# Optimization experiments

Hardware: AMD Instinct MI355X
Metric: run time of the kernel (lower is better)

The kernel has to match this reference:

```python
import jax, jax.numpy as jnp
import numpy as np

EPS = 1e-6

def _rmsnorm(x, w):
    var = jnp.mean(x * x, axis=-1, keepdims=True)
    return w * (x * jax.lax.rsqrt(var + EPS))

def _rope(t, cos, sin):
    # t: [B,S,H,d_k]; cos/sin: [S,d_k/2] -> complex multiply on (even,odd) pairs
    B, S, H, D = t.shape
    tr = t.reshape(B, S, H, D // 2, 2)
    t0, t1 = tr[..., 0], tr[..., 1]
    c = cos[None, :, None, :]
    s = sin[None, :, None, :]
    o0 = t0 * c - t1 * s
    o1 = t0 * s + t1 * c
    return jnp.stack([o0, o1], axis=-1).reshape(B, S, H, D)

def setup_inputs() -> dict:
    key = jax.random.key(0)
    ks = jax.random.split(key, 9)
    B, S, D, H, DFF = 1, 4096, 1024, 16, 4096
    dk = D // H
    hidden = int(2 * DFF / 3)  # 2730, SwiGLU hidden dim
    sc = 0.02
    x = jax.random.normal(ks[0], (B, S, D), jnp.float32)
    # RoPE tables (theta=10000)
    inv_freq = 1.0 / (10000.0 ** (np.arange(0, dk, 2, dtype=np.float32) / dk))
    ang = np.outer(np.arange(S, dtype=np.float32), inv_freq)
    freqs_cos = jnp.asarray(np.cos(ang))
    freqs_sin = jnp.asarray(np.sin(ang))
    # causal additive mask [1,1,S,S]
    mask = jnp.where(np.tril(np.ones((S, S), bool)), 0.0, -1e9).astype(jnp.float32)[None, None]
    Wq = jax.random.normal(ks[1], (D, D), jnp.float32) * sc
    Wk = jax.random.normal(ks[2], (D, D), jnp.float32) * sc
    Wv = jax.random.normal(ks[3], (D, D), jnp.float32) * sc
    Wo = jax.random.normal(ks[4], (D, D), jnp.float32) * sc
    ln1_w = jnp.ones((D,), jnp.float32)
    ln2_w = jnp.ones((D,), jnp.float32)
    w1 = jax.random.normal(ks[5], (D, hidden), jnp.float32) * sc
    w2 = jax.random.normal(ks[6], (hidden, D), jnp.float32) * sc
    w3 = jax.random.normal(ks[7], (D, hidden), jnp.float32) * sc
    return dict(x=x, freqs_cos=freqs_cos, freqs_sin=freqs_sin, mask=mask,
                Wq=Wq, Wk=Wk, Wv=Wv, Wo=Wo, ln1_w=ln1_w, ln2_w=ln2_w,
                w1=w1, w2=w2, w3=w3)

def reference(x, freqs_cos, freqs_sin, mask, Wq, Wk, Wv, Wo, ln1_w, ln2_w, w1, w2, w3):
    B, S, D = x.shape
    H = 16
    dk = D // H
    scale = jnp.sqrt(jnp.float32(dk))
    # attention sublayer (pre-RMSNorm)
    h = _rmsnorm(x, ln1_w)
    Q = (h @ Wq).reshape(B, S, H, dk)
    K = (h @ Wk).reshape(B, S, H, dk)
    V = (h @ Wv).reshape(B, S, H, dk)
    Q = _rope(Q, freqs_cos, freqs_sin)
    K = _rope(K, freqs_cos, freqs_sin)
    scores = jnp.einsum('bshd,bthd->bhst', Q, K) / scale + mask  # [B,H,S,S]
    attn = jax.nn.softmax(scores, axis=-1)
    ctx = jnp.einsum('bhst,bthd->bshd', attn, V).reshape(B, S, D)
    x = x + ctx @ Wo
    # SwiGLU FFN sublayer
    h2 = _rmsnorm(x, ln2_w)
    ff = (jax.nn.silu(h2 @ w1) * (h2 @ w3)) @ w2
    x = x + ff
    return x
```

## Files before the change

kernel.cpp:

```cpp
#include <hip/hip_runtime.h>

#define S_LEN 4096
#define D_MODEL 1024
#define NHEAD 16
#define DK 64
#define HID 2730
#define HIDP 2880
#define QKV_LD 3072

typedef unsigned short u16;
typedef unsigned int u32;
typedef __bf16 bf16x8 __attribute__((ext_vector_type(8)));
typedef float f32x4 __attribute__((ext_vector_type(4)));

#define MFMA16 __builtin_amdgcn_mfma_f32_16x16x32_bf16
#define EXP2 __builtin_amdgcn_exp2f

__device__ __forceinline__ float b2f(u16 u) {
    return __builtin_bit_cast(float, (u32)u << 16);
}
__device__ __forceinline__ u16 f2b(float f) {
    u32 u = __builtin_bit_cast(u32, f);
    u += 0x7FFF + ((u >> 16) & 1);
    return (u16)(u >> 16);
}
__device__ __forceinline__ u32 pk_trunc(float lo, float hi) {
    return __builtin_amdgcn_perm(__builtin_bit_cast(u32, hi),
                                 __builtin_bit_cast(u32, lo), 0x07060302u);
}
__device__ __forceinline__ void gll16(const u16* g, u16* l) {
    __builtin_amdgcn_global_load_lds(
        (__attribute__((address_space(1))) void*)(g),
        (__attribute__((address_space(3))) void*)(l),
        16, 0, 0);
}

__global__ __launch_bounds__(256)
void prep_k(const float* s0, const float* s1, const float* s2,
            const float* s3, const float* s4, const float* s5,
            const float* s6, u16* d0, u16* d1, u16* d2, u16* d3,
            u16* d4, u16* d5, u16* d6,
            const float* __restrict__ x, const float* __restrict__ ln1,
            u16* __restrict__ hb) {
    __shared__ float t[32][33];
    __shared__ float red[4];
    const int bid = blockIdx.x;
    const int tid = threadIdx.x;

    if (bid >= 12736) {
        const int row = bid - 12736;
        const float4 v = ((const float4*)(x + (size_t)row * D_MODEL))[tid];
        float ss = v.x * v.x + v.y * v.y + v.z * v.z + v.w * v.w;
        for (int o = 32; o; o >>= 1) ss += __shfl_down(ss, o);
        if ((tid & 63) == 0) red[tid >> 6] = ss;
        __syncthreads();
        const float tot = red[0] + red[1] + red[2] + red[3];
        const float rs = rsqrtf(tot * (1.0f / D_MODEL) + 1e-6f);
        const float4 wv = ((const float4*)ln1)[tid];
        u16* op = hb + (size_t)row * D_MODEL + tid * 4;
        u32 p0 = (u32)f2b(v.x * rs * wv.x) | ((u32)f2b(v.y * rs * wv.y) << 16);
        u32 p1 = (u32)f2b(v.z * rs * wv.z) | ((u32)f2b(v.w * rs * wv.w) << 16);
        uint2 pk; pk.x = p0; pk.y = p1;
        *(uint2*)op = pk;
        return;
    }

    const float* srcs[7] = {s0, s1, s2, s3, s4, s5, s6};
    u16* dsts[7] = {d0, d1, d2, d3, d4, d5, d6};
    const int RR[7] = {1024, 1024, 1024, 1024, 1024, 1024, 2730};
    const int CC[7] = {1024, 1024, 1024, 1024, 2730, 2730, 1024};
    const int OC[7] = {1024, 1024, 1024, 1024, 1024, 1024, 2880};
    const int XD[7] = {32, 32, 32, 32, 32, 32, 90};

    int seg, start;
    if (bid < 4096)      { seg = bid >> 10; start = seg << 10; }
    else if (bid < 6976) { seg = 4; start = 4096; }
    else if (bid < 9856) { seg = 5; start = 6976; }
    else                 { seg = 6; start = 9856; }
    const int local = bid - start;
    const int bx = local % XD[seg], byy = local / XD[seg];
    const float* in = srcs[seg];
    u16* out = dsts[seg];
    const int R = RR[seg], C = CC[seg], outC = OC[seg];

    const int r0 = byy * 32;
    const int c0 = bx * 32;
    const int tx = tid & 31, ty = tid >> 5;
#pragma unroll
    for (int j = 0; j < 4; ++j) {
        int ir = c0 + ty + j * 8;
        int ic = r0 + tx;
        t[ty + j * 8][tx] = (ir < R && ic < C) ? in[(size_t)ir * C + ic] : 0.0f;
    }
    __syncthreads();
#pragma unroll
    for (int j = 0; j < 4; ++j)
        out[(size_t)(r0 + ty + j * 8) * outC + c0 + tx] = f2b(t[tx][ty + j * 8]);
}

__global__ __launch_bounds__(256)
void rmsnorm_k(const float* __restrict__ x, const float* __restrict__ w,
               u16* __restrict__ out) {
    const int row = blockIdx.x;
    const int tid = threadIdx.x;
    const float4 v = ((const float4*)(x + (size_t)row * D_MODEL))[tid];
    float ss = v.x * v.x + v.y * v.y + v.z * v.z + v.w * v.w;
    for (int o = 32; o; o >>= 1) ss += __shfl_down(ss, o);
    __shared__ float red[4];
    if ((tid & 63) == 0) red[tid >> 6] = ss;
    __syncthreads();
    const float tot = red[0] + red[1] + red[2] + red[3];
    const float rs = rsqrtf(tot * (1.0f / D_MODEL) + 1e-6f);
    const float4 wv = ((const float4*)w)[tid];
    u16* op = out + (size_t)row * D_MODEL + tid * 4;
    u32 p0 = (u32)f2b(v.x * rs * wv.x) | ((u32)f2b(v.y * rs * wv.y) << 16);
    u32 p1 = (u32)f2b(v.z * rs * wv.z) | ((u32)f2b(v.w * rs * wv.w) << 16);
    uint2 pk; pk.x = p0; pk.y = p1;
    *(uint2*)op = pk;
}

__global__ __launch_bounds__(256)
void packkv_k(const u16* __restrict__ qkv, const float* __restrict__ fc,
              const float* __restrict__ fs, u16* __restrict__ vt,
              u16* __restrict__ kp) {
    __shared__ u16 t[32][33];
    const int h = blockIdx.z;
    const int t0 = blockIdx.x * 32;
    const int d0 = blockIdx.y * 32;
    const int tx = threadIdx.x, ty = threadIdx.y;
#pragma unroll
    for (int j = 0; j < 4; ++j)
        t[ty + j * 8][tx] =
            qkv[(size_t)(t0 + ty + j * 8) * QKV_LD + 2 * D_MODEL + h * DK + d0 + tx];

    const int id = ty * 32 + tx;
    const int sA = t0 + (id >> 3);
    const int dA = d0 + (id & 7) * 4;
    uint2 kvp = *(const uint2*)(qkv + (size_t)sA * QKV_LD + D_MODEL + h * DK + dA);
    const int fi = sA * 32 + (dA >> 1);
    const float cc0 = fc[fi], ss0 = fs[fi];
    const float cc1 = fc[fi + 1], ss1 = fs[fi + 1];
    auto rpk = [](u32 w, float c, float s) -> u32 {
        const float a = b2f((u16)w), b = b2f((u16)(w >> 16));
        return (u32)f2b(a * c - b * s) | ((u32)f2b(a * s + b * c) << 16);
    };
    kvp.x = rpk(kvp.x, cc0, ss0);
    kvp.y = rpk(kvp.y, cc1, ss1);
    *(uint2*)(kp + ((size_t)h * S_LEN + sA) * DK + dA) = kvp;

    __syncthreads();
#pragma unroll
    for (int j = 0; j < 4; ++j)
        vt[(size_t)h * DK * S_LEN + (size_t)(d0 + ty + j * 8) * S_LEN + t0 + tx] =
            t[tx][ty + j * 8];
}

template <int EPI>
__global__ __launch_bounds__(256)
void gemm128(const u16* __restrict__ A, int lda, const u16* __restrict__ Bt, int ldb,
             void* __restrict__ C, int ldc, int K, const float* __restrict__ resid) {
    const int m0 = blockIdx.y * 128, n0 = blockIdx.x * 128;
    const int tid = threadIdx.x;
    const int wave = tid >> 6, lane = tid & 63;
    const int wr = wave >> 1, wc = wave & 1;
    const int r16 = lane & 15, kq = lane >> 4;

    __shared__ __align__(16) u16 As[128 * 64];
    __shared__ __align__(16) u16 Bs[128 * 64];

    const int srow = tid >> 3;
    const int scol = ((tid & 7) ^ (srow & 7)) * 8;
    const u16* ag0 = A + (size_t)(m0 +  0 + srow) * lda + scol;
    const u16* ag1 = A + (size_t)(m0 + 32 + srow) * lda + scol;
    const u16* ag2 = A + (size_t)(m0 + 64 + srow) * lda + scol;
    const u16* ag3 = A + (size_t)(m0 + 96 + srow) * lda + scol;
    const u16* bg0 = Bt + (size_t)(n0 +  0 + srow) * ldb + scol;
    const u16* bg1 = Bt + (size_t)(n0 + 32 + srow) * ldb + scol;
    const u16* bg2 = Bt + (size_t)(n0 + 64 + srow) * ldb + scol;
    const u16* bg3 = Bt + (size_t)(n0 + 96 + srow) * ldb + scol;
    u16* const ad = As + tid * 8;
    u16* const bd = Bs + tid * 8;

    f32x4 acc[16];
#pragma unroll
    for (int i = 0; i < 16; ++i) acc[i] = f32x4{0.f, 0.f, 0.f, 0.f};

    const int rsw = r16 & 7;
    for (int k0 = 0; k0 < K; k0 += 64) {
        __syncthreads();
        gll16(ag0 + k0, ad);
        gll16(ag1 + k0, ad + 2048);
        gll16(ag2 + k0, ad + 4096);
        gll16(ag3 + k0, ad + 6144);
        gll16(bg0 + k0, bd);
        gll16(bg1 + k0, bd + 2048);
        gll16(bg2 + k0, bd + 4096);
        gll16(bg3 + k0, bd + 6144);
        __syncthreads();
#pragma unroll
        for (int ks = 0; ks < 2; ++ks) {
            const int slot = (((ks << 2) | kq) ^ rsw) * 8;
            bf16x8 af[4], bf[4];
#pragma unroll
            for (int mt = 0; mt < 4; ++mt)
                af[mt] = *(const bf16x8*)&As[(wr * 64 + mt * 16 + r16) * 64 + slot];
#pragma unroll
            for (int nt = 0; nt < 4; ++nt)
                bf[nt] = *(const bf16x8*)&Bs[(wc * 64 + nt * 16 + r16) * 64 + slot];
#pragma unroll
            for (int mt = 0; mt < 4; ++mt)
#pragma unroll
                for (int nt = 0; nt < 4; ++nt)
                    acc[mt * 4 + nt] = MFMA16(af[mt], bf[nt], acc[mt * 4 + nt], 0, 0, 0);
        }
    }

#pragma unroll
    for (int mt = 0; mt < 4; ++mt) {
#pragma unroll
        for (int nt = 0; nt < 4; ++nt) {
            const int col = n0 + wc * 64 + nt * 16 + r16;
#pragma unroll
            for (int j = 0; j < 4; ++j) {
                const int row = m0 + wr * 64 + mt * 16 + kq * 4 + j;
                if (EPI == 0) {
                    ((u16*)C)[(size_t)row * ldc + col] = f2b(acc[mt * 4 + nt][j]);
                } else {
                    ((float*)C)[(size_t)row * ldc + col] =
                        resid[(size_t)row * ldc + col] + acc[mt * 4 + nt][j];
                }
            }
        }
    }
}

__global__ __launch_bounds__(256)
void gemm64r(const u16* __restrict__ A, int lda, const u16* __restrict__ Bt, int ldb,
             float* __restrict__ C, int ldc, int K, const float* __restrict__ resid) {
    const int m0 = blockIdx.y * 128, n0 = blockIdx.x * 64;
    const int tid = threadIdx.x;
    const int wave = tid >> 6, lane = tid & 63;
    const int r16 = lane & 15, kq = lane >> 4;

    __shared__ __align__(16) u16 As[128 * 64];
    __shared__ __align__(16) u16 Bs[64 * 64];

    const int srow = tid >> 3;
    const int scol = ((tid & 7) ^ (srow & 7)) * 8;
    const u16* ag0 = A + (size_t)(m0 +  0 + srow) * lda + scol;
    const u16* ag1 = A + (size_t)(m0 + 32 + srow) * lda + scol;
    const u16* ag2 = A + (size_t)(m0 + 64 + srow) * lda + scol;
    const u16* ag3 = A + (size_t)(m0 + 96 + srow) * lda + scol;
    const u16* bg0 = Bt + (size_t)(n0 +  0 + srow) * ldb + scol;
    const u16* bg1 = Bt + (size_t)(n0 + 32 + srow) * ldb + scol;
    u16* const ad = As + tid * 8;
    u16* const bd = Bs + tid * 8;

    f32x4 acc[8];
#pragma unroll
    for (int i = 0; i < 8; ++i) acc[i] = f32x4{0.f, 0.f, 0.f, 0.f};

    const int rsw = r16 & 7;
    for (int k0 = 0; k0 < K; k0 += 64) {
        __syncthreads();
        gll16(ag0 + k0, ad);
        gll16(ag1 + k0, ad + 2048);
        gll16(ag2 + k0, ad + 4096);
        gll16(ag3 + k0, ad + 6144);
        gll16(bg0 + k0, bd);
        gll16(bg1 + k0, bd + 2048);
        __syncthreads();
#pragma unroll
        for (int ks = 0; ks < 2; ++ks) {
            const int slot = (((ks << 2) | kq) ^ rsw) * 8;
            bf16x8 af[2], bf[4];
#pragma unroll
            for (int mt = 0; mt < 2; ++mt)
                af[mt] = *(const bf16x8*)&As[(wave * 32 + mt * 16 + r16) * 64 + slot];
#pragma unroll
            for (int nt = 0; nt < 4; ++nt)
                bf[nt] = *(const bf16x8*)&Bs[(nt * 16 + r16) * 64 + slot];
#pragma unroll
            for (int mt = 0; mt < 2; ++mt)
#pragma unroll
                for (int nt = 0; nt < 4; ++nt)
                    acc[mt * 4 + nt] = MFMA16(af[mt], bf[nt], acc[mt * 4 + nt], 0, 0, 0);
        }
    }

#pragma unroll
    for (int mt = 0; mt < 2; ++mt)
#pragma unroll
        for (int nt = 0; nt < 4; ++nt) {
            const int col = n0 + nt * 16 + r16;
#pragma unroll
            for (int j = 0; j < 4; ++j) {
                const int row = m0 + wave * 32 + mt * 16 + kq * 4 + j;
                C[(size_t)row * ldc + col] =
                    resid[(size_t)row * ldc + col] + acc[mt * 4 + nt][j];
            }
        }
}

__global__ __launch_bounds__(256, 3)
void gemm_dual96x(const u16* __restrict__ A, int lda,
                  const u16* __restrict__ B1, const u16* __restrict__ B3, int ldb,
                  u16* __restrict__ C, int ldc, int K) {
    const int m0 = blockIdx.y * 128, n0 = blockIdx.x * 96;
    const int tid = threadIdx.x;
    const int wave = tid >> 6, lane = tid & 63;
    const int wr = wave >> 1, wc = wave & 1;
    const int r16 = lane & 15, kq = lane >> 4;

    __shared__ __align__(16) u16 As[128 * 64];
    __shared__ __align__(16) u16 Bs[192 * 64];

    const int srow = tid >> 3;
    const int scol = ((tid & 7) ^ (srow & 7)) * 8;
    const u16* ag0 = A + (size_t)(m0 +  0 + srow) * lda + scol;
    const u16* ag1 = A + (size_t)(m0 + 32 + srow) * lda + scol;
    const u16* ag2 = A + (size_t)(m0 + 64 + srow) * lda + scol;
    const u16* ag3 = A + (size_t)(m0 + 96 + srow) * lda + scol;
    const u16* bg0 = B1 + (size_t)(n0 +  0 + srow) * ldb + scol;
    const u16* bg1 = B1 + (size_t)(n0 + 32 + srow) * ldb + scol;
    const u16* bg2 = B1 + (size_t)(n0 + 64 + srow) * ldb + scol;
    const u16* bg3 = B3 + (size_t)(n0 +  0 + srow) * ldb + scol;
    const u16* bg4 = B3 + (size_t)(n0 + 32 + srow) * ldb + scol;
    const u16* bg5 = B3 + (size_t)(n0 + 64 + srow) * ldb + scol;
    u16* const ad = As + tid * 8;
    u16* const bd = Bs + tid * 8;

    f32x4 acc1[12], acc3[12];
#pragma unroll
    for (int i = 0; i < 12; ++i) {
        acc1[i] = f32x4{0.f, 0.f, 0.f, 0.f};
        acc3[i] = f32x4{0.f, 0.f, 0.f, 0.f};
    }

    const int rsw = r16 & 7;
    for (int k0 = 0; k0 < K; k0 += 64) {
        __syncthreads();
        gll16(ag0 + k0, ad);
        gll16(ag1 + k0, ad + 2048);
        gll16(ag2 + k0, ad + 4096);
        gll16(ag3 + k0, ad + 6144);
        gll16(bg0 + k0, bd);
        gll16(bg1 + k0, bd + 2048);
        gll16(bg2 + k0, bd + 4096);
        gll16(bg3 + k0, bd + 6144);
        gll16(bg4 + k0, bd + 8192);
        gll16(bg5 + k0, bd + 10240);
        __syncthreads();
#pragma unroll
        for (int ks = 0; ks < 2; ++ks) {
            const int slot = (((ks << 2) | kq) ^ rsw) * 8;
            bf16x8 af[4], b1f[3], b3f[3];
#pragma unroll
            for (int mt = 0; mt < 4; ++mt)
                af[mt] = *(const bf16x8*)&As[(wr * 64 + mt * 16 + r16) * 64 + slot];
#pragma unroll
            for (int nt = 0; nt < 3; ++nt) {
                b1f[nt] = *(const bf16x8*)&Bs[(wc * 48 + nt * 16 + r16) * 64 + slot];
                b3f[nt] = *(const bf16x8*)&Bs[(96 + wc * 48 + nt * 16 + r16) * 64 + slot];
            }
#pragma unroll
            for (int mt = 0; mt < 4; ++mt)
#pragma unroll
                for (int nt = 0; nt < 3; ++nt) {
                    acc1[mt * 3 + nt] = MFMA16(af[mt], b1f[nt], acc1[mt * 3 + nt], 0, 0, 0);
                    acc3[mt * 3 + nt] = MFMA16(af[mt], b3f[nt], acc3[mt * 3 + nt], 0, 0, 0);
                }
        }
    }

#pragma unroll
    for (int mt = 0; mt < 4; ++mt)
#pragma unroll
        for (int nt = 0; nt < 3; ++nt) {
            const int col = n0 + wc * 48 + nt * 16 + r16;
#pragma unroll
            for (int j = 0; j < 4; ++j) {
                const int row = m0 + wr * 64 + mt * 16 + kq * 4 + j;
                const float v1 = acc1[mt * 3 + nt][j];
                const float v3 = acc3[mt * 3 + nt][j];
                const float sig = 1.0f / (1.0f + __expf(-v1));
                C[(size_t)row * ldc + col] = f2b(v1 * sig * v3);
            }
        }
}

__global__ __launch_bounds__(256)
void flash_k(const u16* __restrict__ qkv, const u16* __restrict__ vt,
             const u16* __restrict__ kp, const float* __restrict__ fc,
             const float* __restrict__ fs, u16* __restrict__ ctx) {
    const int h = blockIdx.x;
    const int pair = blockIdx.y;
    const int qa = pair, qb = 63 - pair;
    const int tid = threadIdx.x;
    const int wave = tid >> 6, lane = tid & 63;
    const int r16 = lane & 15, kq = lane >> 4;

    __shared__ __align__(16) u16 Kb[2][2 * 64 * 64];
    __shared__ __align__(16) u16 Vb[2][2 * 64 * 64];
    __shared__ __align__(16) u16 PsB[4 * 16 * 64];
    __shared__ __align__(16) u16 PsA[4 * 16 * 64];

    const u16* kb = kp + (size_t)h * S_LEN * DK;
    const u16* vb = vt + (size_t)h * DK * S_LEN;
    const int srow = tid >> 3;
    const int lcol = ((tid & 7) ^ (srow & 7)) * 8;
    const int qloc = wave * 16 + r16;
    const int sw = r16 & 7;
    const int c0 = (kq ^ sw) * 8;
    const int c1 = ((4 ^ kq) ^ sw) * 8;
    const int psw = r16 & 14;
    u16* psB = PsB + wave * 1024 + r16 * 64;
    u16* psA = PsA + wave * 1024 + r16 * 64;

    const float SC = 0.125f * 1.44269504f;
    auto rp = [SC](u32 w, float c, float s) -> u32 {
        const float a = b2f((u16)w), b = b2f((u16)(w >> 16));
        return (u32)f2b((a * c - b * s) * SC) |
               ((u32)f2b((a * s + b * c) * SC) << 16);
    };
    auto loadq = [&](int qglob, bf16x8& q0out, bf16x8& q1out) {
        const u16* qrow = qkv + (size_t)qglob * QKV_LD + h * DK;
        uint4 uq0 = *(const uint4*)(qrow + kq * 8);
        uint4 uq1 = *(const uint4*)(qrow + 32 + kq * 8);
        const float4 c0v = *(const float4*)(fc + qglob * 32 + kq * 4);
        const float4 s0v = *(const float4*)(fs + qglob * 32 + kq * 4);
        const float4 c1v = *(const float4*)(fc + qglob * 32 + 16 + kq * 4);
        const float4 s1v = *(const float4*)(fs + qglob * 32 + 16 + kq * 4);
        uq0.x = rp(uq0.x, c0v.x, s0v.x); uq0.y = rp(uq0.y, c0v.y, s0v.y);
        uq0.z = rp(uq0.z, c0v.z, s0v.z); uq0.w = rp(uq0.w, c0v.w, s0v.w);
        uq1.x = rp(uq1.x, c1v.x, s1v.x); uq1.y = rp(uq1.y, c1v.y, s1v.y);
        uq1.z = rp(uq1.z, c1v.z, s1v.z); uq1.w = rp(uq1.w, c1v.w, s1v.w);
        q0out = __builtin_bit_cast(bf16x8, uq0);
        q1out = __builtin_bit_cast(bf16x8, uq1);
    };
    const int qgA = qa * 64 + qloc;
    const int qgB = qb * 64 + qloc;
    bf16x8 qfA0, qfA1, qfB0, qfB1;
    loadq(qgA, qfA0, qfA1);
    loadq(qgB, qfB0, qfB1);

    f32x4 oA[4], oB[4];
#pragma unroll
    for (int i = 0; i < 4; ++i) {
        oA[i] = f32x4{0.f, 0.f, 0.f, 0.f};
        oB[i] = f32x4{0.f, 0.f, 0.f, 0.f};
    }
    f32x4 laccA = f32x4{0.f, 0.f, 0.f, 0.f};
    f32x4 laccB = f32x4{0.f, 0.f, 0.f, 0.f};
    const uint4 uone = make_uint4(0x3F803F80u, 0x3F803F80u, 0x3F803F80u, 0x3F803F80u);
    const bf16x8 ones = __builtin_bit_cast(bf16x8, uone);

    auto tile_single = [&](const u16* Ks, const u16* Vs, bool dmask) {
        f32x4 s[4];
#pragma unroll
        for (int nt = 0; nt < 4; ++nt) {
            s[nt] = f32x4{0.f, 0.f, 0.f, 0.f};
            const bf16x8 k0 = *(const bf16x8*)&Ks[(nt * 16 + r16) * 64 + c0];
            s[nt] = MFMA16(k0, qfB0, s[nt], 0, 0, 0);
            const bf16x8 k1 = *(const bf16x8*)&Ks[(nt * 16 + r16) * 64 + c1];
            s[nt] = MFMA16(k1, qfB1, s[nt], 0, 0, 0);
        }
        float pr[16];
#pragma unroll
        for (int nt = 0; nt < 4; ++nt)
#pragma unroll
            for (int j = 0; j < 4; ++j) pr[nt * 4 + j] = EXP2(s[nt][j]);
        if (dmask) {
#pragma unroll
            for (int nt = 0; nt < 4; ++nt)
#pragma unroll
                for (int j = 0; j < 4; ++j)
                    if ((nt * 16 + kq * 4 + j) > qloc) pr[nt * 4 + j] = 0.f;
        }
#pragma unroll
        for (int nt = 0; nt < 4; ++nt) {
            uint2 pk;
            pk.x = pk_trunc(pr[nt * 4 + 0], pr[nt * 4 + 1]);
            pk.y = pk_trunc(pr[nt * 4 + 2], pr[nt * 4 + 3]);
            *(uint2*)&psB[((nt * 4 + kq) ^ psw) * 4] = pk;
        }
#pragma unroll
        for (int ks = 0; ks < 2; ++ks) {
            const bf16x8 pf = *(const bf16x8*)&psB[((8 * ks + 2 * kq) ^ psw) * 4];
            laccB = MFMA16(ones, pf, laccB, 0, 0, 0);
            const int cv = (((ks << 2) ^ kq) ^ sw) * 8;
#pragma unroll
            for (int nt = 0; nt < 4; ++nt) {
                const bf16x8 vf = *(const bf16x8*)&Vs[(nt * 16 + r16) * 64 + cv];
                oB[nt] = MFMA16(vf, pf, oB[nt], 0, 0, 0);
            }
        }
    };

    auto tile_dual = [&](const u16* Ks, const u16* Vs, bool maskA) {
        f32x4 sB[4], sA[4];
#pragma unroll
        for (int nt = 0; nt < 4; ++nt) {
            sB[nt] = f32x4{0.f, 0.f, 0.f, 0.f};
            sA[nt] = f32x4{0.f, 0.f, 0.f, 0.f};
            const bf16x8 k0 = *(const bf16x8*)&Ks[(nt * 16 + r16) * 64 + c0];
            sB[nt] = MFMA16(k0, qfB0, sB[nt], 0, 0, 0);
            sA[nt] = MFMA16(k0, qfA0, sA[nt], 0, 0, 0);
            const bf16x8 k1 = *(const bf16x8*)&Ks[(nt * 16 + r16) * 64 + c1];
            sB[nt] = MFMA16(k1, qfB1, sB[nt], 0, 0, 0);
            sA[nt] = MFMA16(k1, qfA1, sA[nt], 0, 0, 0);
        }
        float prB[16], prA[16];
#pragma unroll
        for (int nt = 0; nt < 4; ++nt)
#pragma unroll
            for (int j = 0; j < 4; ++j) {
                prB[nt * 4 + j] = EXP2(sB[nt][j]);
                prA[nt * 4 + j] = EXP2(sA[nt][j]);
            }
        if (maskA) {
#pragma unroll
            for (int nt = 0; nt < 4; ++nt)
#pragma unroll
                for (int j = 0; j < 4; ++j)
                    if ((nt * 16 + kq * 4 + j) > qloc) prA[nt * 4 + j] = 0.f;
        }
#pragma unroll
        for (int nt = 0; nt < 4; ++nt) {
            uint2 pkB, pkA;
            pkB.x = pk_trunc(prB[nt * 4 + 0], prB[nt * 4 + 1]);
            pkB.y = pk_trunc(prB[nt * 4 + 2], prB[nt * 4 + 3]);
            pkA.x = pk_trunc(prA[nt * 4 + 0], prA[nt * 4 + 1]);
            pkA.y = pk_trunc(prA[nt * 4 + 2], prA[nt * 4 + 3]);
            *(uint2*)&psB[((nt * 4 + kq) ^ psw) * 4] = pkB;
            *(uint2*)&psA[((nt * 4 + kq) ^ psw) * 4] = pkA;
        }
#pragma unroll
        for (int ks = 0; ks < 2; ++ks) {
            const bf16x8 pfB = *(const bf16x8*)&psB[((8 * ks + 2 * kq) ^ psw) * 4];
            const bf16x8 pfA = *(const bf16x8*)&psA[((8 * ks + 2 * kq) ^ psw) * 4];
            laccB = MFMA16(ones, pfB, laccB, 0, 0, 0);
            laccA = MFMA16(ones, pfA, laccA, 0, 0, 0);
            const int cv = (((ks << 2) ^ kq) ^ sw) * 8;
#pragma unroll
            for (int nt = 0; nt < 4; ++nt) {
                const bf16x8 vf = *(const bf16x8*)&Vs[(nt * 16 + r16) * 64 + cv];
                oB[nt] = MFMA16(vf, pfB, oB[nt], 0, 0, 0);
                oA[nt] = MFMA16(vf, pfA, oA[nt], 0, 0, 0);
            }
        }
    };

    auto stage = [&](int t, u16* kd, u16* vd) {
        const int tb = t * 64;
#pragma unroll
        for (int i = 0; i < 2; ++i) {
            const int r = srow + i * 32;
            gll16(kb + (size_t)(tb + r) * DK + lcol, kd + tid * 8 + i * 2048);
            gll16(vb + (size_t)r * S_LEN + tb + lcol, vd + tid * 8 + i * 2048);
        }
    };

    stage(0, Kb[0], Vb[0]);
    stage(1, Kb[0] + 4096, Vb[0] + 4096);

    const int nT = (qb + 2) >> 1;
    for (int T = 0; T < nT; ++T) {
        __syncthreads();
        const int nb = (T + 1) * 2;
        if (nb <= qb) {
            u16* kd = ((T + 1) & 1) ? Kb[1] : Kb[0];
            u16* vd = ((T + 1) & 1) ? Vb[1] : Vb[0];
            stage(nb, kd, vd);
            if (nb + 1 <= qb) stage(nb + 1, kd + 4096, vd + 4096);
        }
        const u16* Ks = (T & 1) ? Kb[1] : Kb[0];
        const u16* Vs = (T & 1) ? Vb[1] : Vb[0];

        {
            const int t = 2 * T;
            if (t <= qa) tile_dual(Ks, Vs, t == qa);
            else         tile_single(Ks, Vs, t == qb);
        }
        if (2 * T + 1 <= qb) {
            const int t = 2 * T + 1;
            if (t <= qa) tile_dual(Ks + 4096, Vs + 4096, t == qa);
            else         tile_single(Ks + 4096, Vs + 4096, t == qb);
        }
    }

    auto wout = [&](f32x4 (&o)[4], float lsum, int qg) {
        const float inv = 1.0f / lsum;
        const size_t row = qg;
#pragma unroll
        for (int nt = 0; nt < 4; ++nt) {
            uint2 pk;
            pk.x = (u32)f2b(o[nt][0] * inv) | ((u32)f2b(o[nt][1] * inv) << 16);
            pk.y = (u32)f2b(o[nt][2] * inv) | ((u32)f2b(o[nt][3] * inv) << 16);
            *(uint2*)&ctx[row * D_MODEL + h * DK + nt * 16 + kq * 4] = pk;
        }
    };
    wout(oA, laccA[0], qgA);
    wout(oB, laccB[0], qgB);
}

extern "C" void kernel_launch(void* const* d_in, const int* in_sizes, int n_in,
                              void* d_out, int out_size, void* d_ws, size_t ws_size,
                              hipStream_t stream) {
    const float* x    = (const float*)d_in[0];
    const float* fcos = (const float*)d_in[1];
    const float* fsin = (const float*)d_in[2];
    const float* Wq = (const float*)d_in[4];
    const float* Wk = (const float*)d_in[5];
    const float* Wv = (const float*)d_in[6];
    const float* Wo = (const float*)d_in[7];
    const float* ln1 = (const float*)d_in[8];
    const float* ln2 = (const float*)d_in[9];
    const float* w1 = (const float*)d_in[10];
    const float* w2 = (const float*)d_in[11];
    const float* w3 = (const float*)d_in[12];
    float* out = (float*)d_out;

    char* ws = (char*)d_ws;
    size_t off = 0;
    auto alloc = [&](size_t bytes) -> char* {
        char* p = ws + off;
        off += (bytes + 255) & ~(size_t)255;
        return p;
    };
    u16* hb    = (u16*)alloc((size_t)S_LEN * D_MODEL * 2);
    u16* wqkvt = (u16*)alloc((size_t)QKV_LD * D_MODEL * 2);
    u16* wot   = (u16*)alloc((size_t)D_MODEL * D_MODEL * 2);
    u16* qkvb  = (u16*)alloc((size_t)S_LEN * QKV_LD * 2);
    u16* vt    = (u16*)alloc((size_t)S_LEN * D_MODEL * 2);
    u16* kpack = (u16*)alloc((size_t)S_LEN * D_MODEL * 2);
    u16* ctxb  = (u16*)alloc((size_t)S_LEN * D_MODEL * 2);
    float* x2  = (float*)alloc((size_t)S_LEN * D_MODEL * 4);
    u16* h2b   = (u16*)alloc((size_t)S_LEN * D_MODEL * 2);
    u16* w1t   = (u16*)alloc((size_t)HIDP * D_MODEL * 2);
    u16* w3t   = (u16*)alloc((size_t)HIDP * D_MODEL * 2);
    u16* w2t   = (u16*)alloc((size_t)D_MODEL * HIDP * 2);
    u16* ffb   = (u16*)alloc((size_t)S_LEN * HIDP * 2);

    const dim3 tb32(32, 8);

    prep_k<<<16832, 256, 0, stream>>>(
        Wq, Wk, Wv, Wo, w1, w3, w2,
        wqkvt, wqkvt + (size_t)D_MODEL * D_MODEL,
        wqkvt + (size_t)2 * D_MODEL * D_MODEL, wot, w1t, w3t, w2t,
        x, ln1, hb);

    gemm128<0><<<dim3(QKV_LD / 128, S_LEN / 128), 256, 0, stream>>>(
        hb, D_MODEL, wqkvt, D_MODEL, qkvb, QKV_LD, D_MODEL, nullptr);

    packkv_k<<<dim3(S_LEN / 32, DK / 32, NHEAD), tb32, 0, stream>>>(
        qkvb, fcos, fsin, vt, kpack);

    flash_k<<<dim3(NHEAD, 32), 256, 0, stream>>>(qkvb, vt, kpack, fcos, fsin, ctxb);

    gemm64r<<<dim3(D_MODEL / 64, S_LEN / 128), 256, 0, stream>>>(
        ctxb, D_MODEL, wot, D_MODEL, x2, D_MODEL, D_MODEL, x);

    rmsnorm_k<<<S_LEN, 256, 0, stream>>>(x2, ln2, h2b);

    gemm_dual96x<<<dim3(HIDP / 96, S_LEN / 128), 256, 0, stream>>>(
        h2b, D_MODEL, w1t, w3t, D_MODEL, ffb, HIDP, D_MODEL);

    gemm64r<<<dim3(D_MODEL / 64, S_LEN / 128), 256, 0, stream>>>(
        ffb, HIDP, w2t, HIDP, out, D_MODEL, HIDP, x2);
}
```

Before: 385.0 us.

## Fuse K RoPE packing and V transpose into the QKV GEMM epilogue

Removes the separate packkv kernel. The QKV GEMM epilogue now writes Q directly, applies RoPE to K using lane shuffles and stores it head-packed, and transposes V through shared memory into the V^T layout. This drops one launch and a full re-read of K/V from global memory. In exchange the epilogue takes on more LDS use (a larger shared buffer) and strided K stores.

```diff
diff --git a/kernel.cpp b/kernel.cpp
--- a/kernel.cpp
+++ b/kernel.cpp
@@ -120,53 +120,19 @@
 }
 
 __global__ __launch_bounds__(256)
-void packkv_k(const u16* __restrict__ qkv, const float* __restrict__ fc,
-              const float* __restrict__ fs, u16* __restrict__ vt,
-              u16* __restrict__ kp) {
-    __shared__ u16 t[32][33];
-    const int h = blockIdx.z;
-    const int t0 = blockIdx.x * 32;
-    const int d0 = blockIdx.y * 32;
-    const int tx = threadIdx.x, ty = threadIdx.y;
-#pragma unroll
-    for (int j = 0; j < 4; ++j)
-        t[ty + j * 8][tx] =
-            qkv[(size_t)(t0 + ty + j * 8) * QKV_LD + 2 * D_MODEL + h * DK + d0 + tx];
-
-    const int id = ty * 32 + tx;
-    const int sA = t0 + (id >> 3);
-    const int dA = d0 + (id & 7) * 4;
-    uint2 kvp = *(const uint2*)(qkv + (size_t)sA * QKV_LD + D_MODEL + h * DK + dA);
-    const int fi = sA * 32 + (dA >> 1);
-    const float cc0 = fc[fi], ss0 = fs[fi];
-    const float cc1 = fc[fi + 1], ss1 = fs[fi + 1];
-    auto rpk = [](u32 w, float c, float s) -> u32 {
-        const float a = b2f((u16)w), b = b2f((u16)(w >> 16));
-        return (u32)f2b(a * c - b * s) | ((u32)f2b(a * s + b * c) << 16);
-    };
-    kvp.x = rpk(kvp.x, cc0, ss0);
-    kvp.y = rpk(kvp.y, cc1, ss1);
-    *(uint2*)(kp + ((size_t)h * S_LEN + sA) * DK + dA) = kvp;
-
-    __syncthreads();
-#pragma unroll
-    for (int j = 0; j < 4; ++j)
-        vt[(size_t)h * DK * S_LEN + (size_t)(d0 + ty + j * 8) * S_LEN + t0 + tx] =
-            t[tx][ty + j * 8];
-}
-
-template <int EPI>
-__global__ __launch_bounds__(256)
-void gemm128(const u16* __restrict__ A, int lda, const u16* __restrict__ Bt, int ldb,
-             void* __restrict__ C, int ldc, int K, const float* __restrict__ resid) {
+void gemm_qkv(const u16* __restrict__ A, int lda, const u16* __restrict__ Bt, int ldb,
+              u16* __restrict__ C, int ldc, int K,
+              const float* __restrict__ fc, const float* __restrict__ fs,
+              u16* __restrict__ kp, u16* __restrict__ vtb) {
     const int m0 = blockIdx.y * 128, n0 = blockIdx.x * 128;
     const int tid = threadIdx.x;
     const int wave = tid >> 6, lane = tid & 63;
     const int wr = wave >> 1, wc = wave & 1;
     const int r16 = lane & 15, kq = lane >> 4;
 
-    __shared__ __align__(16) u16 As[128 * 64];
-    __shared__ __align__(16) u16 Bs[128 * 64];
+    __shared__ __align__(16) u16 S[128 * 136];
+    u16* const As = S;
+    u16* const Bs = S + 8192;
 
     const int srow = tid >> 3;
     const int scol = ((tid & 7) ^ (srow & 7)) * 8;
@@ -215,21 +181,63 @@
         }
     }
 
-#pragma unroll
-    for (int mt = 0; mt < 4; ++mt) {
-#pragma unroll
-        for (int nt = 0; nt < 4; ++nt) {
-            const int col = n0 + wc * 64 + nt * 16 + r16;
-#pragma unroll
-            for (int j = 0; j < 4; ++j) {
-                const int row = m0 + wr * 64 + mt * 16 + kq * 4 + j;
-                if (EPI == 0) {
-                    ((u16*)C)[(size_t)row * ldc + col] = f2b(acc[mt * 4 + nt][j]);
-                } else {
-                    ((float*)C)[(size_t)row * ldc + col] =
-                        resid[(size_t)row * ldc + col] + acc[mt * 4 + nt][j];
+    if (n0 < D_MODEL) {
+#pragma unroll
+        for (int mt = 0; mt < 4; ++mt)
+#pragma unroll
+            for (int nt = 0; nt < 4; ++nt) {
+                const int col = n0 + wc * 64 + nt * 16 + r16;
+#pragma unroll
+                for (int j = 0; j < 4; ++j) {
+                    const int row = m0 + wr * 64 + mt * 16 + kq * 4 + j;
+                    C[(size_t)row * ldc + col] = f2b(acc[mt * 4 + nt][j]);
                 }
             }
+    } else if (n0 < 2 * D_MODEL) {
+#pragma unroll
+        for (int mt = 0; mt < 4; ++mt)
+#pragma unroll
+            for (int nt = 0; nt < 4; ++nt) {
+                const int kcol = n0 - D_MODEL + wc * 64 + nt * 16 + r16;
+                const int h = kcol >> 6, d = kcol & 63;
+#pragma unroll
+                for (int j = 0; j < 4; ++j) {
+                    const int row = m0 + wr * 64 + mt * 16 + kq * 4 + j;
+                    const float v = acc[mt * 4 + nt][j];
+                    const float p = __shfl_xor(v, 1);
+                    const int fi = row * 32 + (d >> 1);
+                    const float cc = fc[fi], ss = fs[fi];
+                    const float o = (d & 1) ? (p * ss + v * cc) : (v * cc - p * ss);
+                    kp[((size_t)h * S_LEN + row) * DK + d] = f2b(o);
+                }
+            }
+    } else {
+        __syncthreads();
+#pragma unroll
+        for (int mt = 0; mt < 4; ++mt)
+#pragma unroll
+            for (int nt = 0; nt < 4; ++nt) {
+                const int dl = wc * 64 + nt * 16 + r16;
+                const int sl = wr * 64 + mt * 16 + kq * 4;
+                uint2 pk;
+                pk.x = (u32)f2b(acc[mt * 4 + nt][0]) |
+                       ((u32)f2b(acc[mt * 4 + nt][1]) << 16);
+                pk.y = (u32)f2b(acc[mt * 4 + nt][2]) |
+                       ((u32)f2b(acc[mt * 4 + nt][3]) << 16);
+                *(uint2*)&S[dl * 136 + sl] = pk;
+            }
+        __syncthreads();
+#pragma unroll
+        for (int it = 0; it < 4; ++it) {
+            const int dl = wave * 8 + (lane >> 3) + it * 32;
+            const int so = (lane & 7) * 16;
+            const uint4 a = *(const uint4*)&S[dl * 136 + so];
+            const uint4 b = *(const uint4*)&S[dl * 136 + so + 8];
+            const int vcol = n0 - 2 * D_MODEL + dl;
+            const int h = vcol >> 6, d = vcol & 63;
+            u16* dst = vtb + (size_t)h * DK * S_LEN + (size_t)d * S_LEN + m0 + so;
+            *(uint4*)dst = a;
+            *(uint4*)(dst + 8) = b;
         }
     }
 }
@@ -642,19 +650,15 @@
     u16* w2t   = (u16*)alloc((size_t)D_MODEL * HIDP * 2);
     u16* ffb   = (u16*)alloc((size_t)S_LEN * HIDP * 2);
 
-    const dim3 tb32(32, 8);
-
     prep_k<<<16832, 256, 0, stream>>>(
         Wq, Wk, Wv, Wo, w1, w3, w2,
         wqkvt, wqkvt + (size_t)D_MODEL * D_MODEL,
         wqkvt + (size_t)2 * D_MODEL * D_MODEL, wot, w1t, w3t, w2t,
         x, ln1, hb);
 
-    gemm128<0><<<dim3(QKV_LD / 128, S_LEN / 128), 256, 0, stream>>>(
-        hb, D_MODEL, wqkvt, D_MODEL, qkvb, QKV_LD, D_MODEL, nullptr);
-
-    packkv_k<<<dim3(S_LEN / 32, DK / 32, NHEAD), tb32, 0, stream>>>(
-        qkvb, fcos, fsin, vt, kpack);
+    gemm_qkv<<<dim3(QKV_LD / 128, S_LEN / 128), 256, 0, stream>>>(
+        hb, D_MODEL, wqkvt, D_MODEL, qkvb, QKV_LD, D_MODEL,
+        fcos, fsin, kpack, vt);
 
     flash_k<<<dim3(NHEAD, 32), 256, 0, stream>>>(qkvb, vt, kpack, fcos, fsin, ctxb);
 
```

New measurement: 383.1 us. Within noise of the previous version (-0.5%).
